# Performance work log

Hardware: AMD Instinct MI355X
Metric: run time of the kernel (lower is better)

Reference implementation:

```python
import jax, jax.numpy as jnp
import numpy as np

E, D, F = 16, 1024, 2048  # num_experts, d_model, d_ff
B, N = 2, 2048
LN_EPS = 1e-5


def setup_inputs() -> dict:
    key = jax.random.key(0)
    ks = jax.random.split(key, 8)
    s = 0.02
    return {
        "x": jax.random.normal(ks[0], (B, N, D), dtype=jnp.float32),
        "router_w": jax.random.normal(ks[1], (E, D), dtype=jnp.float32) * s,   # torch Linear weight [out,in]
        "router_b": jnp.zeros((E,), dtype=jnp.float32),
        "w1": jax.random.normal(ks[2], (E, F, D), dtype=jnp.float32) * s,      # SwiGLU w1 per expert
        "w2": jax.random.normal(ks[3], (E, D, F), dtype=jnp.float32) * s,      # SwiGLU w2 per expert
        "w3": jax.random.normal(ks[4], (E, F, D), dtype=jnp.float32) * s,      # SwiGLU w3 per expert
        "ln_g": jnp.ones((E, D), dtype=jnp.float32),                           # per-expert LayerNorm gamma
        "ln_b": jnp.zeros((E, D), dtype=jnp.float32),                          # per-expert LayerNorm beta
    }


def reference(x, router_w, router_b, w1, w2, w3, ln_g, ln_b):
    """SparseMixtureOfExperts.forward (eval mode: no router noise, dropout=0).

    Top-2 routing over softmax(router logits), renormalized; each selected
    expert applies LayerNorm(SwiGLU(x)). Exact math of the torch masked loop,
    expressed as a scan over experts with zero coefficients for unrouted tokens.
    """
    Bx, Nx, Dx = x.shape
    xf = x.reshape(-1, Dx)  # [T, D]

    logits = xf @ router_w.T + router_b              # [T, E]
    probs = jax.nn.softmax(logits, axis=-1)
    top_w, top_e = jax.lax.top_k(probs, 2)           # [T, 2]
    top_w = top_w / jnp.sum(top_w, axis=-1, keepdims=True)

    def body(acc, params):
        W1, W2, W3, gm, bt, eid = params
        h = jax.nn.silu(xf @ W1.T) * (xf @ W3.T)     # [T, F]
        y = h @ W2.T                                 # [T, D]
        mu = jnp.mean(y, axis=-1, keepdims=True)
        var = jnp.var(y, axis=-1, keepdims=True)     # biased, matches torch LayerNorm
        yn = (y - mu) / jnp.sqrt(var + LN_EPS) * gm + bt
        # combined routing coefficient over both top-2 slots for this expert
        coeff = jnp.sum(jnp.where(top_e == eid, top_w, 0.0), axis=-1)  # [T]
        return acc + coeff[:, None] * yn, None

    eids = jnp.arange(router_w.shape[0], dtype=top_e.dtype)
    out, _ = jax.lax.scan(body, jnp.zeros_like(xf), (w1, w2, w3, ln_g, ln_b, eids))
    return out.reshape(Bx, Nx, Dx)
```

## Files before the change

kernel.cpp:

```cpp
#include <hip/hip_runtime.h>
#include <hip/hip_bf16.h>

#define T_TOK 4096
#define DM    1024
#define FF    2048
#define NE    16
#define NP    8192
#define LS    56

typedef __bf16 bf16x8 __attribute__((ext_vector_type(8)));
typedef float  f32x4  __attribute__((ext_vector_type(4)));

static __device__ __forceinline__ unsigned short f2bf(float f) {
    union { float f; unsigned u; } v; v.f = f;
    unsigned r = v.u + 0x7fffu + ((v.u >> 16) & 1u);
    return (unsigned short)(r >> 16);
}

static __device__ __forceinline__ ushort4 f4tobf(float4 v) {
    ushort4 c; c.x = f2bf(v.x); c.y = f2bf(v.y); c.z = f2bf(v.z); c.w = f2bf(v.w);
    return c;
}

__global__ __launch_bounds__(256) void k_router(
    const float* __restrict__ x, const float* __restrict__ rw,
    const float* __restrict__ rb, unsigned short* __restrict__ xb,
    int* __restrict__ e0a, int* __restrict__ e1a,
    float* __restrict__ w0a, float* __restrict__ w1a, int* __restrict__ counts)
{
    const int t = blockIdx.x, tid = threadIdx.x;
    float4 xv = ((const float4*)(x + (size_t)t * DM))[tid];
    ((ushort4*)(xb + (size_t)t * DM))[tid] = f4tobf(xv);
    float part[NE];
#pragma unroll
    for (int e = 0; e < NE; ++e) {
        float4 wv = ((const float4*)(rw + (size_t)e * DM))[tid];
        part[e] = xv.x*wv.x + xv.y*wv.y + xv.z*wv.z + xv.w*wv.w;
    }
#pragma unroll
    for (int e = 0; e < NE; ++e) {
        float v = part[e];
#pragma unroll
        for (int off = 32; off > 0; off >>= 1) v += __shfl_down(v, off);
        part[e] = v;
    }
    __shared__ float red[4][NE];
    const int lane = tid & 63, wv_ = tid >> 6;
    if (lane == 0) {
#pragma unroll
        for (int e = 0; e < NE; ++e) red[wv_][e] = part[e];
    }
    __syncthreads();
    if (tid == 0) {
        float lg[NE];
#pragma unroll
        for (int e = 0; e < NE; ++e)
            lg[e] = red[0][e] + red[1][e] + red[2][e] + red[3][e] + rb[e];
        int b0 = 0;
        for (int e = 1; e < NE; ++e) if (lg[e] > lg[b0]) b0 = e;
        int b1 = (b0 == 0) ? 1 : 0;
        for (int e = 0; e < NE; ++e) { if (e == b0) continue; if (lg[e] > lg[b1]) b1 = e; }
        float m  = fmaxf(lg[b0], lg[b1]);
        float x0 = __expf(lg[b0] - m), x1 = __expf(lg[b1] - m);
        float inv = 1.f / (x0 + x1);
        e0a[t] = b0; e1a[t] = b1; w0a[t] = x0 * inv; w1a[t] = x1 * inv;
        atomicAdd(&counts[b0], 1); atomicAdd(&counts[b1], 1);
    }
}

__global__ void k_scan(const int* __restrict__ counts, int* __restrict__ offs)
{
    if (threadIdx.x == 0) {
        int s = 0;
        for (int e = 0; e < NE; ++e) { offs[e] = s; s += counts[e]; }
        offs[NE] = s;
    }
}

__global__ __launch_bounds__(256) void k_scatter(
    const int* __restrict__ e0a, const int* __restrict__ e1a,
    const int* __restrict__ offs, int* __restrict__ cursors,
    int* __restrict__ p0a, int* __restrict__ p1a, int* __restrict__ pair_tok)
{
    const int t = blockIdx.x * 256 + threadIdx.x;
    if (t >= T_TOK) return;
    int e0 = e0a[t];
    int p = offs[e0] + atomicAdd(&cursors[e0], 1);
    pair_tok[p] = t; p0a[t] = p;
    int e1 = e1a[t];
    p = offs[e1] + atomicAdd(&cursors[e1], 1);
    pair_tok[p] = t; p1a[t] = p;
}

__global__ __launch_bounds__(512) void k_ffn1(
    const unsigned short* __restrict__ xb, const float* __restrict__ w1g,
    const float* __restrict__ w3g, const int* __restrict__ pair_tok,
    const int* __restrict__ offs, const int* __restrict__ counts,
    unsigned short* __restrict__ h)
{
    const int e = blockIdx.z;
    const int cnt = counts[e];
    const int m0 = blockIdx.x * 128;
    if (m0 >= cnt) return;
    const int base = offs[e];
    const int n0 = blockIdx.y * 128;
    const float* __restrict__ W1 = w1g + (size_t)e * FF * DM;
    const float* __restrict__ W3 = w3g + (size_t)e * FF * DM;

    __shared__ __attribute__((aligned(16))) unsigned short As[128][LS];
    __shared__ __attribute__((aligned(16))) unsigned short B1s[128][LS];
    __shared__ __attribute__((aligned(16))) unsigned short B3s[128][LS];

    const int tid = threadIdx.x;
    const int ar = tid >> 2, aseg = tid & 3;
    const int tok = pair_tok[base + min(m0 + ar, cnt - 1)];
    const unsigned short* __restrict__ xrow = xb + (size_t)tok * DM + aseg * 8;

    const int br = tid >> 3, bseg = tid & 7;
    const float* __restrict__ W1r0 = W1 + (size_t)(n0 + br) * DM + bseg * 4;
    const float* __restrict__ W1r1 = W1 + (size_t)(n0 + br + 64) * DM + bseg * 4;
    const float* __restrict__ W3r0 = W3 + (size_t)(n0 + br) * DM + bseg * 4;
    const float* __restrict__ W3r1 = W3 + (size_t)(n0 + br + 64) * DM + bseg * 4;

    const int wave = tid >> 6, lane = tid & 63;
    const int wm = (wave >> 2) * 64, wn = (wave & 3) * 32;
    const int lr = lane & 15, lk = (lane >> 4) * 8;

    f32x4 acc1[4][2], acc3[4][2];
#pragma unroll
    for (int i = 0; i < 4; ++i)
#pragma unroll
        for (int j = 0; j < 2; ++j) {
            acc1[i][j] = f32x4{0.f, 0.f, 0.f, 0.f};
            acc3[i][j] = f32x4{0.f, 0.f, 0.f, 0.f};
        }

    for (int k0 = 0; k0 < DM; k0 += 32) {
        *(uint4*)&As[ar][aseg * 8] = *(const uint4*)(xrow + k0);
        float4 a0 = *(const float4*)(W1r0 + k0);
        float4 a1 = *(const float4*)(W1r1 + k0);
        float4 c0 = *(const float4*)(W3r0 + k0);
        float4 c1 = *(const float4*)(W3r1 + k0);
        *(ushort4*)&B1s[br][bseg * 4]      = f4tobf(a0);
        *(ushort4*)&B1s[br + 64][bseg * 4] = f4tobf(a1);
        *(ushort4*)&B3s[br][bseg * 4]      = f4tobf(c0);
        *(ushort4*)&B3s[br + 64][bseg * 4] = f4tobf(c1);
        __syncthreads();
        bf16x8 af[4], b1f[2], b3f[2];
#pragma unroll
        for (int i = 0; i < 4; ++i) af[i] = *(const bf16x8*)&As[wm + i*16 + lr][lk];
#pragma unroll
        for (int j = 0; j < 2; ++j) {
            b1f[j] = *(const bf16x8*)&B1s[wn + j*16 + lr][lk];
            b3f[j] = *(const bf16x8*)&B3s[wn + j*16 + lr][lk];
        }
#pragma unroll
        for (int i = 0; i < 4; ++i)
#pragma unroll
            for (int j = 0; j < 2; ++j) {
                acc1[i][j] = __builtin_amdgcn_mfma_f32_16x16x32_bf16(af[i], b1f[j], acc1[i][j], 0, 0, 0);
                acc3[i][j] = __builtin_amdgcn_mfma_f32_16x16x32_bf16(af[i], b3f[j], acc3[i][j], 0, 0, 0);
            }
        __syncthreads();
    }
    const int orb = (lane >> 4) * 4, oc = lane & 15;
#pragma unroll
    for (int i = 0; i < 4; ++i) {
#pragma unroll
        for (int r = 0; r < 4; ++r) {
            int m = m0 + wm + i*16 + orb + r;
            if (m < cnt) {
                size_t prow = (size_t)(base + m) * FF + n0 + wn;
#pragma unroll
                for (int j = 0; j < 2; ++j) {
                    float a = acc1[i][j][r], c = acc3[i][j][r];
                    float hv = (a / (1.f + __expf(-a))) * c;
                    h[prow + j*16 + oc] = f2bf(hv);
                }
            }
        }
    }
}

__global__ __launch_bounds__(512) void k_ffn2(
    const unsigned short* __restrict__ h, const float* __restrict__ w2g,
    const int* __restrict__ offs, const int* __restrict__ counts,
    float* __restrict__ y)
{
    const int e = blockIdx.z;
    const int cnt = counts[e];
    const int m0 = blockIdx.x * 128;
    if (m0 >= cnt) return;
    const int base = offs[e];
    const int n0 = blockIdx.y * 128;
    const float* __restrict__ W2 = w2g + (size_t)e * DM * FF;

    __shared__ __attribute__((aligned(16))) unsigned short As[128][LS];
    __shared__ __attribute__((aligned(16))) unsigned short Bs[128][LS];

    const int tid = threadIdx.x;
    const int ar = tid >> 2, aseg = tid & 3;
    const size_t arow = (size_t)min(base + m0 + ar, NP - 1) * FF + aseg * 8;

    const int br = tid >> 3, bseg = tid & 7;
    const float* __restrict__ W2r0 = W2 + (size_t)(n0 + br) * FF + bseg * 4;
    const float* __restrict__ W2r1 = W2 + (size_t)(n0 + br + 64) * FF + bseg * 4;

    const int wave = tid >> 6, lane = tid & 63;
    const int wm = (wave >> 2) * 64, wn = (wave & 3) * 32;
    const int lr = lane & 15, lk = (lane >> 4) * 8;

    f32x4 acc[4][2];
#pragma unroll
    for (int i = 0; i < 4; ++i)
#pragma unroll
        for (int j = 0; j < 2; ++j) acc[i][j] = f32x4{0.f, 0.f, 0.f, 0.f};

    for (int k0 = 0; k0 < FF; k0 += 32) {
        *(uint4*)&As[ar][aseg * 8] = *(const uint4*)(h + arow + k0);
        float4 v0 = *(const float4*)(W2r0 + k0);
        float4 v1 = *(const float4*)(W2r1 + k0);
        *(ushort4*)&Bs[br][bseg * 4]      = f4tobf(v0);
        *(ushort4*)&Bs[br + 64][bseg * 4] = f4tobf(v1);
        __syncthreads();
        bf16x8 af[4], bf[2];
#pragma unroll
        for (int i = 0; i < 4; ++i) af[i] = *(const bf16x8*)&As[wm + i*16 + lr][lk];
#pragma unroll
        for (int j = 0; j < 2; ++j) bf[j] = *(const bf16x8*)&Bs[wn + j*16 + lr][lk];
#pragma unroll
        for (int i = 0; i < 4; ++i)
#pragma unroll
            for (int j = 0; j < 2; ++j)
                acc[i][j] = __builtin_amdgcn_mfma_f32_16x16x32_bf16(af[i], bf[j], acc[i][j], 0, 0, 0);
        __syncthreads();
    }
    const int orb = (lane >> 4) * 4, oc = lane & 15;
#pragma unroll
    for (int i = 0; i < 4; ++i) {
#pragma unroll
        for (int r = 0; r < 4; ++r) {
            int m = m0 + wm + i*16 + orb + r;
            if (m < cnt) {
                size_t yrow = (size_t)(base + m) * DM + n0 + wn;
#pragma unroll
                for (int j = 0; j < 2; ++j) y[yrow + j*16 + oc] = acc[i][j][r];
            }
        }
    }
}

__global__ __launch_bounds__(256) void k_ln(
    const float* __restrict__ y, const int* __restrict__ p0a, const int* __restrict__ p1a,
    const int* __restrict__ e0a, const int* __restrict__ e1a,
    const float* __restrict__ w0a, const float* __restrict__ w1a,
    const float* __restrict__ lng, const float* __restrict__ lnb,
    float* __restrict__ out)
{
    const int t = blockIdx.x, tid = threadIdx.x;
    const int p0 = p0a[t], p1 = p1a[t], e0 = e0a[t], e1 = e1a[t];
    const float cw0 = w0a[t], cw1 = w1a[t];
    float4 y0 = ((const float4*)(y + (size_t)p0 * DM))[tid];
    float4 y1 = ((const float4*)(y + (size_t)p1 * DM))[tid];
    float s0 = y0.x + y0.y + y0.z + y0.w;
    float q0 = y0.x*y0.x + y0.y*y0.y + y0.z*y0.z + y0.w*y0.w;
    float s1 = y1.x + y1.y + y1.z + y1.w;
    float q1 = y1.x*y1.x + y1.y*y1.y + y1.z*y1.z + y1.w*y1.w;
#pragma unroll
    for (int off = 32; off > 0; off >>= 1) {
        s0 += __shfl_down(s0, off); q0 += __shfl_down(q0, off);
        s1 += __shfl_down(s1, off); q1 += __shfl_down(q1, off);
    }
    __shared__ float rbuf[4][4];
    const int lane = tid & 63, wv_ = tid >> 6;
    if (lane == 0) { rbuf[wv_][0] = s0; rbuf[wv_][1] = q0; rbuf[wv_][2] = s1; rbuf[wv_][3] = q1; }
    __syncthreads();
    float S0 = rbuf[0][0] + rbuf[1][0] + rbuf[2][0] + rbuf[3][0];
    float Q0 = rbuf[0][1] + rbuf[1][1] + rbuf[2][1] + rbuf[3][1];
    float S1 = rbuf[0][2] + rbuf[1][2] + rbuf[2][2] + rbuf[3][2];
    float Q1 = rbuf[0][3] + rbuf[1][3] + rbuf[2][3] + rbuf[3][3];
    const float invD = 1.f / (float)DM;
    float mu0 = S0 * invD, mu1 = S1 * invD;
    float rs0 = rsqrtf(fmaxf(Q0 * invD - mu0 * mu0, 0.f) + 1e-5f);
    float rs1 = rsqrtf(fmaxf(Q1 * invD - mu1 * mu1, 0.f) + 1e-5f);
    float4 g0 = ((const float4*)(lng + (size_t)e0 * DM))[tid];
    float4 b0 = ((const float4*)(lnb + (size_t)e0 * DM))[tid];
    float4 g1 = ((const float4*)(lng + (size_t)e1 * DM))[tid];
    float4 b1 = ((const float4*)(lnb + (size_t)e1 * DM))[tid];
    float4 o;
    o.x = cw0 * ((y0.x - mu0) * rs0 * g0.x + b0.x) + cw1 * ((y1.x - mu1) * rs1 * g1.x + b1.x);
    o.y = cw0 * ((y0.y - mu0) * rs0 * g0.y + b0.y) + cw1 * ((y1.y - mu1) * rs1 * g1.y + b1.y);
    o.z = cw0 * ((y0.z - mu0) * rs0 * g0.z + b0.z) + cw1 * ((y1.z - mu1) * rs1 * g1.z + b1.z);
    o.w = cw0 * ((y0.w - mu0) * rs0 * g0.w + b0.w) + cw1 * ((y1.w - mu1) * rs1 * g1.w + b1.w);
    ((float4*)(out + (size_t)t * DM))[tid] = o;
}

extern "C" void kernel_launch(void* const* d_in, const int* in_sizes, int n_in,
                              void* d_out, int out_size, void* d_ws, size_t ws_size,
                              hipStream_t stream)
{
    const float* x   = (const float*)d_in[0];
    const float* rw  = (const float*)d_in[1];
    const float* rb  = (const float*)d_in[2];
    const float* w1  = (const float*)d_in[3];
    const float* w2  = (const float*)d_in[4];
    const float* w3  = (const float*)d_in[5];
    const float* lng = (const float*)d_in[6];
    const float* lnb = (const float*)d_in[7];
    float* out = (float*)d_out;
    char* ws = (char*)d_ws;

    const size_t OFF_XB   = 0;
    const size_t OFF_H    = OFF_XB + (size_t)T_TOK * DM * 2;
    const size_t OFF_Y    = OFF_H + (size_t)NP * FF * 2;
    const size_t OFF_META = OFF_Y + (size_t)NP * DM * 4;

    unsigned short* xb = (unsigned short*)(ws + OFF_XB);
    unsigned short* h  = (unsigned short*)(ws + OFF_H);
    float* y           = (float*)(ws + OFF_Y);
    int* counts   = (int*)(ws + OFF_META);
    int* cursors  = counts + 16;
    int* offs     = counts + 32;
    int* e0a      = (int*)(ws + OFF_META + 256);
    int* e1a      = e0a + T_TOK;
    float* w0a    = (float*)(e1a + T_TOK);
    float* w1a    = w0a + T_TOK;
    int* p0a      = (int*)(w1a + T_TOK);
    int* p1a      = p0a + T_TOK;
    int* pair_tok = p1a + T_TOK;

    hipMemsetAsync(ws + OFF_META, 0, 128, stream);
    k_router<<<T_TOK, 256, 0, stream>>>(x, rw, rb, xb, e0a, e1a, w0a, w1a, counts);
    k_scan<<<1, 64, 0, stream>>>(counts, offs);
    k_scatter<<<T_TOK / 256, 256, 0, stream>>>(e0a, e1a, offs, cursors, p0a, p1a, pair_tok);
    k_ffn1<<<dim3(32, FF / 128, NE), 512, 0, stream>>>(xb, w1, w3, pair_tok, offs, counts, h);
    k_ffn2<<<dim3(32, DM / 128, NE), 512, 0, stream>>>(h, w2, offs, counts, y);
    k_ln<<<T_TOK, 256, 0, stream>>>(y, p0a, p1a, e0a, e1a, w0a, w1a, lng, lnb, out);
}
```

Baseline: 1.676 ms.

## Pre-convert expert weights to bf16 and use async LDS-loading double-buffered GEMMs

Adds a conversion pass that turns all w1/w3/w2 expert weights from fp32 into bf16 workspace copies on every call. New FFN kernels then stream bf16 tiles straight into LDS with global_load_lds, double-buffered over K, and feed 16x16x32 bf16 MFMAs. The goal is to cut the fp32 weight traffic and the in-kernel conversion and staging cost inside the GEMMs. In exchange it adds a full read of 384MB of fp32 weights plus a 192MB bf16 write per call, and it needs a larger workspace, otherwise it falls back to the old kernels.

Measured after the change: 1.514 ms. 1.11x faster.

```diff
diff --git a/kernel.cpp b/kernel.cpp
--- a/kernel.cpp
+++ b/kernel.cpp
@@ -20,6 +20,22 @@
 static __device__ __forceinline__ ushort4 f4tobf(float4 v) {
     ushort4 c; c.x = f2bf(v.x); c.y = f2bf(v.y); c.z = f2bf(v.z); c.w = f2bf(v.w);
     return c;
+}
+
+#define GLOAD16(gp, lp) \
+    __builtin_amdgcn_global_load_lds((const __attribute__((address_space(1))) unsigned*)(gp), \
+                                     (__attribute__((address_space(3))) unsigned*)(lp), 16, 0, 0)
+
+__global__ __launch_bounds__(256) void k_convert(
+    const float* __restrict__ s, unsigned short* __restrict__ d, int n8)
+{
+    for (int i = blockIdx.x * 256 + threadIdx.x; i < n8; i += gridDim.x * 256) {
+        const float4* sp = (const float4*)s + (size_t)i * 2;
+        float4 a = sp[0], b = sp[1];
+        union { ushort4 u4[2]; uint4 v; } w;
+        w.u4[0] = f4tobf(a); w.u4[1] = f4tobf(b);
+        ((uint4*)d)[i] = w.v;
+    }
 }
 
 __global__ __launch_bounds__(256) void k_router(
@@ -90,6 +106,164 @@
     int e1 = e1a[t];
     p = offs[e1] + atomicAdd(&cursors[e1], 1);
     pair_tok[p] = t; p1a[t] = p;
+}
+
+__global__ __launch_bounds__(512) void k_ffn1b(
+    const unsigned short* __restrict__ xb, const unsigned short* __restrict__ w1b,
+    const unsigned short* __restrict__ w3b, const int* __restrict__ pair_tok,
+    const int* __restrict__ offs, const int* __restrict__ counts,
+    unsigned short* __restrict__ h)
+{
+    const int e = blockIdx.z;
+    const int cnt = counts[e];
+    const int m0 = blockIdx.x * 128;
+    if (m0 >= cnt) return;
+    const int base = offs[e];
+    const int n0 = blockIdx.y * 128;
+
+    __shared__ __attribute__((aligned(16))) unsigned short As[2][128 * 32];
+    __shared__ __attribute__((aligned(16))) unsigned short B1s[2][128 * 32];
+    __shared__ __attribute__((aligned(16))) unsigned short B3s[2][128 * 32];
+
+    const int tid = threadIdx.x;
+    const int srow = tid >> 2, sseg = tid & 3;
+    const int tok = pair_tok[base + min(m0 + srow, cnt - 1)];
+    const unsigned short* gA  = xb  + (size_t)tok * DM + sseg * 8;
+    const unsigned short* gB1 = w1b + (size_t)e * FF * DM + (size_t)(n0 + srow) * DM + sseg * 8;
+    const unsigned short* gB3 = w3b + (size_t)e * FF * DM + (size_t)(n0 + srow) * DM + sseg * 8;
+
+    const int wave = tid >> 6, lane = tid & 63;
+    const int wm = (wave >> 2) * 64, wn = (wave & 3) * 32;
+    const int lr = lane & 15, lk = (lane >> 4) * 8;
+
+    f32x4 acc1[4][2], acc3[4][2];
+#pragma unroll
+    for (int i = 0; i < 4; ++i)
+#pragma unroll
+        for (int j = 0; j < 2; ++j) {
+            acc1[i][j] = f32x4{0.f, 0.f, 0.f, 0.f};
+            acc3[i][j] = f32x4{0.f, 0.f, 0.f, 0.f};
+        }
+
+    GLOAD16(gA,  &As [0][tid * 8]);
+    GLOAD16(gB1, &B1s[0][tid * 8]);
+    GLOAD16(gB3, &B3s[0][tid * 8]);
+    __syncthreads();
+
+    int cur = 0;
+    for (int k0 = 32; k0 <= DM; k0 += 32) {
+        if (k0 < DM) {
+            const int nxt = cur ^ 1;
+            GLOAD16(gA  + k0, &As [nxt][tid * 8]);
+            GLOAD16(gB1 + k0, &B1s[nxt][tid * 8]);
+            GLOAD16(gB3 + k0, &B3s[nxt][tid * 8]);
+        }
+        bf16x8 af[4], b1f[2], b3f[2];
+#pragma unroll
+        for (int i = 0; i < 4; ++i) af[i] = *(const bf16x8*)&As[cur][(wm + i*16 + lr) * 32 + lk];
+#pragma unroll
+        for (int j = 0; j < 2; ++j) {
+            b1f[j] = *(const bf16x8*)&B1s[cur][(wn + j*16 + lr) * 32 + lk];
+            b3f[j] = *(const bf16x8*)&B3s[cur][(wn + j*16 + lr) * 32 + lk];
+        }
+#pragma unroll
+        for (int i = 0; i < 4; ++i)
+#pragma unroll
+            for (int j = 0; j < 2; ++j) {
+                acc1[i][j] = __builtin_amdgcn_mfma_f32_16x16x32_bf16(af[i], b1f[j], acc1[i][j], 0, 0, 0);
+                acc3[i][j] = __builtin_amdgcn_mfma_f32_16x16x32_bf16(af[i], b3f[j], acc3[i][j], 0, 0, 0);
+            }
+        __syncthreads();
+        cur ^= 1;
+    }
+
+    const int orb = (lane >> 4) * 4, oc = lane & 15;
+#pragma unroll
+    for (int i = 0; i < 4; ++i) {
+#pragma unroll
+        for (int r = 0; r < 4; ++r) {
+            int m = m0 + wm + i*16 + orb + r;
+            if (m < cnt) {
+                size_t prow = (size_t)(base + m) * FF + n0 + wn;
+#pragma unroll
+                for (int j = 0; j < 2; ++j) {
+                    float a = acc1[i][j][r], c = acc3[i][j][r];
+                    float hv = (a / (1.f + __expf(-a))) * c;
+                    h[prow + j*16 + oc] = f2bf(hv);
+                }
+            }
+        }
+    }
+}
+
+__global__ __launch_bounds__(512) void k_ffn2b(
+    const unsigned short* __restrict__ h, const unsigned short* __restrict__ w2b,
+    const int* __restrict__ offs, const int* __restrict__ counts,
+    float* __restrict__ y)
+{
+    const int e = blockIdx.z;
+    const int cnt = counts[e];
+    const int m0 = blockIdx.x * 128;
+    if (m0 >= cnt) return;
+    const int base = offs[e];
+    const int n0 = blockIdx.y * 128;
+
+    __shared__ __attribute__((aligned(16))) unsigned short As[2][128 * 32];
+    __shared__ __attribute__((aligned(16))) unsigned short Bs[2][128 * 32];
+
+    const int tid = threadIdx.x;
+    const int srow = tid >> 2, sseg = tid & 3;
+    const unsigned short* gA = h + (size_t)min(base + m0 + srow, NP - 1) * FF + sseg * 8;
+    const unsigned short* gB = w2b + (size_t)e * DM * FF + (size_t)(n0 + srow) * FF + sseg * 8;
+
+    const int wave = tid >> 6, lane = tid & 63;
+    const int wm = (wave >> 2) * 64, wn = (wave & 3) * 32;
+    const int lr = lane & 15, lk = (lane >> 4) * 8;
+
+    f32x4 acc[4][2];
+#pragma unroll
+    for (int i = 0; i < 4; ++i)
+#pragma unroll
+        for (int j = 0; j < 2; ++j) acc[i][j] = f32x4{0.f, 0.f, 0.f, 0.f};
+
+    GLOAD16(gA, &As[0][tid * 8]);
+    GLOAD16(gB, &Bs[0][tid * 8]);
+    __syncthreads();
+
+    int cur = 0;
+    for (int k0 = 32; k0 <= FF; k0 += 32) {
+        if (k0 < FF) {
+            const int nxt = cur ^ 1;
+            GLOAD16(gA + k0, &As[nxt][tid * 8]);
+            GLOAD16(gB + k0, &Bs[nxt][tid * 8]);
+        }
+        bf16x8 af[4], bf[2];
+#pragma unroll
+        for (int i = 0; i < 4; ++i) af[i] = *(const bf16x8*)&As[cur][(wm + i*16 + lr) * 32 + lk];
+#pragma unroll
+        for (int j = 0; j < 2; ++j) bf[j] = *(const bf16x8*)&Bs[cur][(wn + j*16 + lr) * 32 + lk];
+#pragma unroll
+        for (int i = 0; i < 4; ++i)
+#pragma unroll
+            for (int j = 0; j < 2; ++j)
+                acc[i][j] = __builtin_amdgcn_mfma_f32_16x16x32_bf16(af[i], bf[j], acc[i][j], 0, 0, 0);
+        __syncthreads();
+        cur ^= 1;
+    }
+
+    const int orb = (lane >> 4) * 4, oc = lane & 15;
+#pragma unroll
+    for (int i = 0; i < 4; ++i) {
+#pragma unroll
+        for (int r = 0; r < 4; ++r) {
+            int m = m0 + wm + i*16 + orb + r;
+            if (m < cnt) {
+                size_t yrow = (size_t)(base + m) * DM + n0 + wn;
+#pragma unroll
+                for (int j = 0; j < 2; ++j) y[yrow + j*16 + oc] = acc[i][j][r];
+            }
+        }
+    }
 }
 
 __global__ __launch_bounds__(512) void k_ffn1(
@@ -314,6 +488,11 @@
     const size_t OFF_H    = OFF_XB + (size_t)T_TOK * DM * 2;
     const size_t OFF_Y    = OFF_H + (size_t)NP * FF * 2;
     const size_t OFF_META = OFF_Y + (size_t)NP * DM * 4;
+    const size_t OFF_W1B  = OFF_META + (1u << 20);
+    const size_t WBYTES   = (size_t)NE * FF * DM * 2;
+    const size_t OFF_W3B  = OFF_W1B + WBYTES;
+    const size_t OFF_W2B  = OFF_W3B + WBYTES;
+    const size_t NEED     = OFF_W2B + WBYTES;
 
     unsigned short* xb = (unsigned short*)(ws + OFF_XB);
     unsigned short* h  = (unsigned short*)(ws + OFF_H);
@@ -333,7 +512,20 @@
     k_router<<<T_TOK, 256, 0, stream>>>(x, rw, rb, xb, e0a, e1a, w0a, w1a, counts);
     k_scan<<<1, 64, 0, stream>>>(counts, offs);
     k_scatter<<<T_TOK / 256, 256, 0, stream>>>(e0a, e1a, offs, cursors, p0a, p1a, pair_tok);
-    k_ffn1<<<dim3(32, FF / 128, NE), 512, 0, stream>>>(xb, w1, w3, pair_tok, offs, counts, h);
-    k_ffn2<<<dim3(32, DM / 128, NE), 512, 0, stream>>>(h, w2, offs, counts, y);
+
+    if (ws_size >= NEED) {
+        unsigned short* w1b = (unsigned short*)(ws + OFF_W1B);
+        unsigned short* w3b = (unsigned short*)(ws + OFF_W3B);
+        unsigned short* w2b = (unsigned short*)(ws + OFF_W2B);
+        const int n8 = NE * FF * DM / 8;
+        k_convert<<<2048, 256, 0, stream>>>(w1, w1b, n8);
+        k_convert<<<2048, 256, 0, stream>>>(w3, w3b, n8);
+        k_convert<<<2048, 256, 0, stream>>>(w2, w2b, n8);
+        k_ffn1b<<<dim3(32, FF / 128, NE), 512, 0, stream>>>(xb, w1b, w3b, pair_tok, offs, counts, h);
+        k_ffn2b<<<dim3(32, DM / 128, NE), 512, 0, stream>>>(h, w2b, offs, counts, y);
+    } else {
+        k_ffn1<<<dim3(32, FF / 128, NE), 512, 0, stream>>>(xb, w1, w3, pair_tok, offs, counts, h);
+        k_ffn2<<<dim3(32, DM / 128, NE), 512, 0, stream>>>(h, w2, offs, counts, y);
+    }
     k_ln<<<T_TOK, 256, 0, stream>>>(y, p0a, p1a, e0a, e1a, w0a, w1a, lng, lnb, out);
 }
```
